# Kernel tuning notes

Hardware: AMD Instinct MI355X
Metric: run time of the kernel (lower is better)

## Reference

```python
import jax, jax.numpy as jnp
import numpy as np

B, T, C = 1, 2048, 1024
H = 16
HD = C // H  # 64
K = 8
EPS = 1e-6
NEG = -1.0e9


def apply_rotary_emb(x, cos, sin):
    # x: (B,T,H,HD), cos/sin: (T, HD//2)
    x1, x2 = jnp.split(x, 2, axis=-1)
    c = cos[None, :, None, :]
    s = sin[None, :, None, :]
    return jnp.concatenate([x1 * c - x2 * s, x1 * s + x2 * c], axis=-1)


def rms_norm(x):
    return x * jax.lax.rsqrt(jnp.mean(jnp.square(x), axis=-1, keepdims=True) + EPS)


def setup_inputs() -> dict:
    key = jax.random.key(0)
    ks = jax.random.split(key, 8)
    x = jax.random.normal(ks[0], (B, T, C), dtype=jnp.float32)
    # standard RoPE tables
    inv_freq = 1.0 / (10000.0 ** (np.arange(0, HD, 2, dtype=np.float32) / HD))
    t = np.arange(T, dtype=np.float32)
    freqs = np.outer(t, inv_freq)  # (T, HD//2)
    cos = jnp.asarray(np.cos(freqs), dtype=jnp.float32)
    sin = jnp.asarray(np.sin(freqs), dtype=jnp.float32)
    std = 0.02
    Wq = std * jax.random.normal(ks[1], (C, C), dtype=jnp.float32)
    Wk = std * jax.random.normal(ks[2], (C, C), dtype=jnp.float32)
    Wv = std * jax.random.normal(ks[3], (C, C), dtype=jnp.float32)
    Wproj = std * jax.random.normal(ks[4], (C, C), dtype=jnp.float32)
    Wdq = jax.random.normal(ks[5], (C, K), dtype=jnp.float32) / np.sqrt(C)
    Wdk = jax.random.normal(ks[6], (C, K), dtype=jnp.float32) / np.sqrt(C)
    return {"x": x, "cos": cos, "sin": sin, "Wq": Wq, "Wk": Wk, "Wv": Wv,
            "Wproj": Wproj, "Wdq": Wdq, "Wdk": Wdk}


def reference(x, cos, sin, Wq, Wk, Wv, Wproj, Wdq, Wdk):
    b, t, c = x.shape
    q = (x @ Wq).reshape(b, t, H, HD)
    k = (x @ Wk).reshape(b, t, H, HD)
    v = (x @ Wv).reshape(b, t, H, HD)
    q = rms_norm(apply_rotary_emb(q, cos, sin))
    k = rms_norm(apply_rotary_emb(k, cos, sin))

    # digit projections (identical for every head in the source module)
    qd = x @ Wdq  # (B,T,K)
    kd = x @ Wdk  # (B,T,K)
    matches = qd[:, :, None, :] == kd[:, None, :, :]  # (B,Tq,Tk,K)
    prefix = jnp.cumprod(matches.astype(jnp.int32), axis=-1)
    lcp = jnp.sum(prefix, axis=-1)  # (B,Tq,Tk)
    lcp_mask = lcp >= (K - 1)

    causal = jnp.tril(jnp.ones((t, t), dtype=bool))
    combined = causal[None, None, :, :] & lcp_mask[:, None, :, :]  # (B,1->H,Tq,Tk)

    scale = 1.0 / jnp.sqrt(jnp.asarray(HD, x.dtype))
    scores = jnp.einsum('bqhd,bkhd->bhqk', q * scale, k)
    scores = jnp.where(combined, scores, NEG)
    w = jax.nn.softmax(scores, axis=-1)
    y = jnp.einsum('bhqk,bkhd->bqhd', w, v).reshape(b, t, c)
    return y @ Wproj
```

## Files before the change

### kernel.cpp

```cpp
#include <hip/hip_runtime.h>
#include <math.h>

#define T_DIM 2048
#define C_DIM 1024
#define H_NUM 16
#define HD_DIM 64
#define K_LCP 8
#define NEG_VAL -1.0e9f
#define NBLK 256

typedef __bf16 bf16;
typedef __bf16 bf16x4 __attribute__((ext_vector_type(4)));
typedef __bf16 bf16x8 __attribute__((ext_vector_type(8)));
typedef float f32x4 __attribute__((ext_vector_type(4)));
typedef unsigned long long u64;

#define ALOAD(p) __hip_atomic_load((p), __ATOMIC_RELAXED, __HIP_MEMORY_SCOPE_AGENT)
#define ASTORE(p, v) \
  __hip_atomic_store((p), (v), __ATOMIC_RELAXED, __HIP_MEMORY_SCOPE_AGENT)

__device__ __forceinline__ u64 pk2(float lo, float hi) {
  return (u64)__float_as_uint(lo) | ((u64)__float_as_uint(hi) << 32);
}
__device__ __forceinline__ float upk_lo(u64 u) {
  return __uint_as_float((unsigned)u);
}
__device__ __forceinline__ float upk_hi(u64 u) {
  return __uint_as_float((unsigned)(u >> 32));
}

struct Prm {
  const float *x, *cosT, *sinT, *Wq, *Wk, *Wv, *Wproj, *Wdq, *Wdk;
  float* out;
  bf16 *xb, *wqt, *wkt, *wvt, *wpt, *qB, *kB, *vB;
  float *qd, *kd, *vtsum, *partial;
  int *tilemask, *allmask;
  u64* maskbits;
  float *vmean, *rowout;
  int* flags;
  int* bars;
};

__device__ __forceinline__ void gbar(int* bars, int slot, bool fence) {
  __syncthreads();
  if (threadIdx.x == 0) {
    if (fence) __threadfence();
    int* B = bars + slot * 32;
    const int g = blockIdx.x >> 5;
    int old = __hip_atomic_fetch_add(&B[1 + g], 1, __ATOMIC_RELAXED,
                                     __HIP_MEMORY_SCOPE_AGENT);
    if (old == 31) {
      __hip_atomic_fetch_add(&B[0], 1, __ATOMIC_RELAXED,
                             __HIP_MEMORY_SCOPE_AGENT);
      while (__hip_atomic_load(&B[0], __ATOMIC_RELAXED,
                               __HIP_MEMORY_SCOPE_AGENT) < 8)
        __builtin_amdgcn_s_sleep(8);
      ASTORE(&B[10 + g], 1);
    } else {
      while (ALOAD(&B[10 + g]) == 0) __builtin_amdgcn_s_sleep(8);
    }
    if (fence) __threadfence();
  }
  __syncthreads();
}

template <int TMt, int MI, int NA>
__device__ void gemm_body(bf16* As, bf16* Bs, const bf16* A, const bf16* Bt,
                          void* Cv, int bx, int by, int z, int mode,
                          const float* cosT, const float* sinT, float* vtsum) {
  const int tid = threadIdx.x;
  const int Kd = C_DIM, N = C_DIM;
  const int bm = by * TMt;
  const int bn = bx * 128;
  const int wave = tid >> 6, lane = tid & 63;
  const int lr = lane >> 2;
  const int lc = (lane & 3) * 8;
  bf16* gA = (bf16*)(A + (size_t)(bm + wave * 16 * NA + lr) * Kd + lc);
  bf16* gB = (bf16*)(Bt + (size_t)(bn + wave * 32 + lr) * Kd + lc);
  bf16* lA = As + wave * 512 * NA;
  bf16* lB = Bs + wave * 1024;
  const int wr = (wave >> 1) * (MI * 16);
  const int wc = (wave & 1) * 64;
  const int fm = lane & 15;
  const int fk_ = (lane >> 4) * 8;

  f32x4 acc[MI][4] = {};
  for (int k0 = 0; k0 < Kd; k0 += 32) {
    __syncthreads();
#pragma unroll
    for (int u = 0; u < NA; ++u)
      __builtin_amdgcn_global_load_lds(
          (__attribute__((address_space(1))) void*)(gA + (size_t)u * 16 * Kd + k0),
          (__attribute__((address_space(3))) void*)(lA + u * 512), 16, 0, 0);
#pragma unroll
    for (int u = 0; u < 2; ++u)
      __builtin_amdgcn_global_load_lds(
          (__attribute__((address_space(1))) void*)(gB + (size_t)u * 16 * Kd + k0),
          (__attribute__((address_space(3))) void*)(lB + u * 512), 16, 0, 0);
    __syncthreads();
    bf16x8 af[MI], bfr[4];
#pragma unroll
    for (int i = 0; i < MI; ++i)
      af[i] = *(const bf16x8*)(As + (size_t)(wr + i * 16 + fm) * 32 + fk_);
#pragma unroll
    for (int j = 0; j < 4; ++j)
      bfr[j] = *(const bf16x8*)(Bs + (size_t)(wc + j * 16 + fm) * 32 + fk_);
#pragma unroll
    for (int i = 0; i < MI; ++i)
#pragma unroll
      for (int j = 0; j < 4; ++j)
        acc[i][j] = __builtin_amdgcn_mfma_f32_16x16x32_bf16(af[i], bfr[j],
                                                            acc[i][j], 0, 0, 0);
  }
  const int cq = (lane >> 4) * 4;
  if (mode && z < 2) {
    bf16* C = (bf16*)Cv;
#pragma unroll
    for (int i = 0; i < MI; ++i)
#pragma unroll
      for (int r = 0; r < 4; ++r) {
        const int t = bm + wr + i * 16 + cq + r;
        float c0 = cosT[(size_t)t * 32 + fm], s0 = sinT[(size_t)t * 32 + fm];
        float c1 = cosT[(size_t)t * 32 + 16 + fm];
        float s1 = sinT[(size_t)t * 32 + 16 + fm];
        float a0 = acc[i][0][r], a1 = acc[i][1][r];
        float a2 = acc[i][2][r], a3 = acc[i][3][r];
        float o0 = a0 * c0 - a2 * s0, o2 = a0 * s0 + a2 * c0;
        float o1 = a1 * c1 - a3 * s1, o3 = a1 * s1 + a3 * c1;
        float ss = o0 * o0 + o1 * o1 + o2 * o2 + o3 * o3;
        ss += __shfl_xor(ss, 1);
        ss += __shfl_xor(ss, 2);
        ss += __shfl_xor(ss, 4);
        ss += __shfl_xor(ss, 8);
        float rn = 1.0f / sqrtf(ss * (1.0f / 64.0f) + 1e-6f);
        size_t base = (size_t)t * N + bn + wc + fm;
        C[base + 0] = (bf16)(o0 * rn);
        C[base + 16] = (bf16)(o1 * rn);
        C[base + 32] = (bf16)(o2 * rn);
        C[base + 48] = (bf16)(o3 * rn);
      }
  } else if (mode) {
    bf16* C = (bf16*)Cv;
#pragma unroll
    for (int i = 0; i < MI; ++i)
#pragma unroll
      for (int r = 0; r < 4; ++r) {
        size_t base = (size_t)(bm + wr + i * 16 + cq + r) * N + bn + wc + fm;
#pragma unroll
        for (int j = 0; j < 4; ++j) C[base + j * 16] = (bf16)acc[i][j][r];
      }
    const int kt = (bm + wr) >> 6;
#pragma unroll
    for (int j = 0; j < 4; ++j) {
      float s = 0.f;
#pragma unroll
      for (int i = 0; i < MI; ++i)
#pragma unroll
        for (int r = 0; r < 4; ++r) s += acc[i][j][r];
      s += __shfl_xor(s, 16);
      s += __shfl_xor(s, 32);
      if ((lane >> 4) == 0)
        vtsum[(size_t)kt * C_DIM + bn + wc + j * 16 + fm] = s;
    }
  } else {
    float* C = (float*)Cv;
#pragma unroll
    for (int i = 0; i < MI; ++i)
#pragma unroll
      for (int r = 0; r < 4; ++r) {
        size_t base = (size_t)(bm + wr + i * 16 + cq + r) * N + bn + wc + fm;
#pragma unroll
        for (int j = 0; j < 4; ++j) C[base + j * 16] = acc[i][j][r];
      }
  }
}

__device__ inline void write_vmean16(const float* vmp, bf16* yp) {
  f32x4 a0 = ((const f32x4*)vmp)[0];
  f32x4 a1 = ((const f32x4*)vmp)[1];
  f32x4 a2 = ((const f32x4*)vmp)[2];
  f32x4 a3 = ((const f32x4*)vmp)[3];
  bf16x8 o0 = {(bf16)a0[0], (bf16)a0[1], (bf16)a0[2], (bf16)a0[3],
               (bf16)a1[0], (bf16)a1[1], (bf16)a1[2], (bf16)a1[3]};
  bf16x8 o1 = {(bf16)a2[0], (bf16)a2[1], (bf16)a2[2], (bf16)a2[3],
               (bf16)a3[0], (bf16)a3[1], (bf16)a3[2], (bf16)a3[3]};
  *(bf16x8*)yp = o0;
  *(bf16x8*)(yp + 8) = o1;
}

__device__ void attn_body(int q64, int h, const bf16* q, const bf16* k,
                          const bf16* v, const float* vtsum,
                          const float* vmean, const u64* maskbits,
                          const int* tilemask, const int* allmask,
                          const int* pneed, bf16* y, char* smem) {
  bf16 (*vsT)[72] = (bf16(*)[72])smem;
  bf16 (*ps)[16][72] = (bf16(*)[16][72])(smem + 9216);
  int (*tmS)[32] = (int(*)[32])(smem + 18432);
  const int q0 = q64 * 64;
  const int tid = threadIdx.x;
  const int wv = tid >> 6;
  const int lane = tid & 63;
  const int qb0 = q0 >> 4;

  const int a0 = allmask[qb0 + 0], a1 = allmask[qb0 + 1];
  const int a2 = allmask[qb0 + 2], a3 = allmask[qb0 + 3];
  const int pn = pneed[q0 >> 6];
  if (a0 & a1 & a2 & a3) {
    if (pn) {
      const int row = tid >> 2, d0 = (tid & 3) * 16;
      write_vmean16(vmean + h * HD_DIM + d0,
                    y + (size_t)(q0 + row) * C_DIM + h * HD_DIM + d0);
    }
    return;
  }
  const int w_active = !((wv == 0) ? a0 : (wv == 1) ? a1 : (wv == 2) ? a2 : a3);

  if (tid < 128)
    tmS[tid >> 5][tid & 31] = tilemask[(size_t)(qb0 + (tid >> 5)) * 32 + (tid & 31)];

  if (!w_active && pn) {
    const int row = wv * 16 + (lane >> 2), d0 = (lane & 3) * 16;
    write_vmean16(vmean + h * HD_DIM + d0,
                  y + (size_t)(q0 + row) * C_DIM + h * HD_DIM + d0);
  }

  const int fm = lane & 15;
  const int fk = (lane >> 4) * 8;
  bf16x8 aq0 = {}, aq1 = {};
  if (w_active) {
    const bf16* qp = q + (size_t)(q0 + wv * 16 + fm) * C_DIM + h * HD_DIM;
    aq0 = *(const bf16x8*)(qp + fk);
    aq1 = *(const bf16x8*)(qp + 32 + fk);
  }
  __syncthreads();

  float m[4] = {-INFINITY, -INFINITY, -INFINITY, -INFINITY};
  float l[4] = {0.f, 0.f, 0.f, 0.f};
  f32x4 out[4] = {};

  for (int kt = 0; kt < T_DIM / 64; ++kt) {
    const int need = tmS[0][kt] | tmS[1][kt] | tmS[2][kt] | tmS[3][kt];
    const int k0 = kt * 64;
    if (need) {
      __syncthreads();
      {
        const int row = tid & 63, d0 = (tid >> 6) * 16;
        const bf16* vp = v + (size_t)(k0 + row) * C_DIM + h * HD_DIM + d0;
        bf16x8 v0 = *(const bf16x8*)(vp);
        bf16x8 v1 = *(const bf16x8*)(vp + 8);
#pragma unroll
        for (int i = 0; i < 8; ++i) vsT[d0 + i][row] = v0[i];
#pragma unroll
        for (int i = 0; i < 8; ++i) vsT[d0 + 8 + i][row] = v1[i];
      }
      __syncthreads();
    }
    if (!w_active) continue;
    if (tmS[wv][kt]) {
      u64 mwr[4];
#pragma unroll
      for (int r = 0; r < 4; ++r)
        mwr[r] = maskbits[(size_t)(q0 + wv * 16 + (lane >> 4) * 4 + r) * 32 + kt] >> fm;
      f32x4 s[4] = {};
#pragma unroll
      for (int j = 0; j < 4; ++j) {
        const bf16* kp = k + (size_t)(k0 + j * 16 + fm) * C_DIM + h * HD_DIM;
        bf16x8 bk0 = *(const bf16x8*)(kp + fk);
        bf16x8 bk1 = *(const bf16x8*)(kp + 32 + fk);
        s[j] = __builtin_amdgcn_mfma_f32_16x16x32_bf16(aq0, bk0, s[j], 0, 0, 0);
        s[j] = __builtin_amdgcn_mfma_f32_16x16x32_bf16(aq1, bk1, s[j], 0, 0, 0);
      }
      float xv[4][4];
      float tmax[4] = {NEG_VAL, NEG_VAL, NEG_VAL, NEG_VAL};
#pragma unroll
      for (int j = 0; j < 4; ++j)
#pragma unroll
        for (int r = 0; r < 4; ++r) {
          float val = ((mwr[r] >> (16 * j)) & 1ull) ? s[j][r] * 0.125f : NEG_VAL;
          xv[j][r] = val;
          tmax[r] = fmaxf(tmax[r], val);
        }
#pragma unroll
      for (int r = 0; r < 4; ++r) {
#pragma unroll
        for (int off = 1; off < 16; off <<= 1)
          tmax[r] = fmaxf(tmax[r], __shfl_xor(tmax[r], off));
      }
      float alpha[4], lsum[4] = {0.f, 0.f, 0.f, 0.f};
#pragma unroll
      for (int r = 0; r < 4; ++r) {
        float mn = fmaxf(m[r], tmax[r]);
        alpha[r] = __expf(m[r] - mn);
        m[r] = mn;
      }
#pragma unroll
      for (int j = 0; j < 4; ++j)
#pragma unroll
        for (int r = 0; r < 4; ++r) {
          float pp = __expf(xv[j][r] - m[r]);
          lsum[r] += pp;
          ps[wv][(lane >> 4) * 4 + r][j * 16 + fm] = (bf16)pp;
        }
#pragma unroll
      for (int r = 0; r < 4; ++r) {
#pragma unroll
        for (int off = 1; off < 16; off <<= 1) lsum[r] += __shfl_xor(lsum[r], off);
        l[r] = l[r] * alpha[r] + lsum[r];
      }
#pragma unroll
      for (int jd = 0; jd < 4; ++jd)
#pragma unroll
        for (int r = 0; r < 4; ++r) out[jd][r] *= alpha[r];
      bf16x8 pa0 = *(const bf16x8*)&ps[wv][fm][fk];
      bf16x8 pa1 = *(const bf16x8*)&ps[wv][fm][32 + fk];
#pragma unroll
      for (int jd = 0; jd < 4; ++jd) {
        bf16x8 bv0 = *(const bf16x8*)&vsT[jd * 16 + fm][fk];
        bf16x8 bv1 = *(const bf16x8*)&vsT[jd * 16 + fm][32 + fk];
        out[jd] = __builtin_amdgcn_mfma_f32_16x16x32_bf16(pa0, bv0, out[jd], 0, 0, 0);
        out[jd] = __builtin_amdgcn_mfma_f32_16x16x32_bf16(pa1, bv1, out[jd], 0, 0, 0);
      }
    } else {
      int needu = (m[0] <= NEG_VAL) | (m[1] <= NEG_VAL) | (m[2] <= NEG_VAL) |
                  (m[3] <= NEG_VAL);
      if (needu) {
#pragma unroll
        for (int jd = 0; jd < 4; ++jd) {
          float vt = vtsum[(size_t)kt * C_DIM + h * HD_DIM + jd * 16 + fm];
#pragma unroll
          for (int r = 0; r < 4; ++r)
            if (m[r] <= NEG_VAL) out[jd][r] += vt;
        }
#pragma unroll
        for (int r = 0; r < 4; ++r)
          if (m[r] <= NEG_VAL) {
            m[r] = NEG_VAL;
            l[r] += 64.f;
          }
      }
    }
  }

  if (w_active) {
#pragma unroll
    for (int r = 0; r < 4; ++r) {
      float inv_l = 1.0f / l[r];
      bf16* yp = y + (size_t)(q0 + wv * 16 + (lane >> 4) * 4 + r) * C_DIM +
                 h * HD_DIM + fm;
#pragma unroll
      for (int jd = 0; jd < 4; ++jd) yp[jd * 16] = (bf16)(out[jd][r] * inv_l);
    }
  }
}

__global__ __launch_bounds__(256, 2) void mono(Prm p) {
  const int gid = blockIdx.x;
  const int tid = threadIdx.x;
  const int wave = tid >> 6, lane = tid & 63;
  __shared__ __align__(16) char smem[19456];

  int* qneed = p.flags;
  int* kneed = p.flags + 16;
  int* vneed = p.flags + 32;
  int* pneed = p.flags + 48;
  int* anyfl = p.flags + 80;

  for (int rr = 0; rr < 2; ++rr) {
    const int t = gid * 8 + rr * 4 + wave;
    const float* xp = p.x + (size_t)t * C_DIM;
    float aq[8] = {}, ak[8] = {};
#pragma unroll
    for (int i = 0; i < 16; ++i) {
      const int c = i * 64 + lane;
      float xv = xp[c];
      float4 wq0 = *(const float4*)(p.Wdq + (size_t)c * K_LCP);
      float4 wq1 = *(const float4*)(p.Wdq + (size_t)c * K_LCP + 4);
      float4 wk0 = *(const float4*)(p.Wdk + (size_t)c * K_LCP);
      float4 wk1 = *(const float4*)(p.Wdk + (size_t)c * K_LCP + 4);
      aq[0] = fmaf(xv, wq0.x, aq[0]); aq[1] = fmaf(xv, wq0.y, aq[1]);
      aq[2] = fmaf(xv, wq0.z, aq[2]); aq[3] = fmaf(xv, wq0.w, aq[3]);
      aq[4] = fmaf(xv, wq1.x, aq[4]); aq[5] = fmaf(xv, wq1.y, aq[5]);
      aq[6] = fmaf(xv, wq1.z, aq[6]); aq[7] = fmaf(xv, wq1.w, aq[7]);
      ak[0] = fmaf(xv, wk0.x, ak[0]); ak[1] = fmaf(xv, wk0.y, ak[1]);
      ak[2] = fmaf(xv, wk0.z, ak[2]); ak[3] = fmaf(xv, wk0.w, ak[3]);
      ak[4] = fmaf(xv, wk1.x, ak[4]); ak[5] = fmaf(xv, wk1.y, ak[5]);
      ak[6] = fmaf(xv, wk1.z, ak[6]); ak[7] = fmaf(xv, wk1.w, ak[7]);
    }
#pragma unroll
    for (int j = 0; j < 8; ++j) {
#pragma unroll
      for (int off = 32; off >= 1; off >>= 1) {
        aq[j] += __shfl_xor(aq[j], off);
        ak[j] += __shfl_xor(ak[j], off);
      }
    }
    if (lane == 0) {
      u64* qdp = (u64*)(p.qd + (size_t)t * K_LCP);
      u64* kdp = (u64*)(p.kd + (size_t)t * K_LCP);
#pragma unroll
      for (int j = 0; j < 4; ++j) {
        ASTORE(qdp + j, pk2(aq[2 * j], aq[2 * j + 1]));
        ASTORE(kdp + j, pk2(ak[2 * j], ak[2 * j + 1]));
      }
    }
  }
  if (gid < 32) {
    f32x4 s = {0.f, 0.f, 0.f, 0.f};
    for (int r = 0; r < 64; ++r)
      s += ((const f32x4*)(p.x + (size_t)(gid * 64 + r) * C_DIM))[tid];
    u64* dst = (u64*)(p.partial + (size_t)gid * C_DIM) + tid * 2;
    ASTORE(dst + 0, pk2(s[0], s[1]));
    ASTORE(dst + 1, pk2(s[2], s[3]));
  }
  gbar(p.bars, 0, false);

  if (gid < 128) {
    const int qb = gid;
    float (*qds)[K_LCP] = (float(*)[K_LCP])smem;
    int* tm = (int*)(smem + 512);
    if (tid < 32) tm[tid] = 0;
    if (tid < 64) {
      u64 u = ALOAD((u64*)(p.qd + (size_t)qb * 16 * K_LCP) + tid);
      qds[tid >> 2][(tid & 3) * 2 + 0] = upk_lo(u);
      qds[tid >> 2][(tid & 3) * 2 + 1] = upk_hi(u);
    }
    __syncthreads();
    const int kmax = qb * 16 + 15;
    for (int it = 0; it < 8; ++it) {
      const int kbase = it * 256 + wave * 64;
      if (kbase > kmax) break;
      const int key = kbase + lane;
      const u64* kp = (const u64*)(p.kd + (size_t)key * K_LCP);
      float kv[K_LCP];
#pragma unroll
      for (int jj = 0; jj < 4; ++jj) {
        u64 u = ALOAD(kp + jj);
        kv[2 * jj + 0] = upk_lo(u);
        kv[2 * jj + 1] = upk_hi(u);
      }
      const int grp = it * 4 + wave;
      u64 anyb = 0ull;
#pragma unroll
      for (int ql = 0; ql < 16; ++ql) {
        const int qg = qb * 16 + ql;
        bool pr = (key <= qg) & (qds[ql][0] == kv[0]) & (qds[ql][1] == kv[1]) &
                  (qds[ql][2] == kv[2]) & (qds[ql][3] == kv[3]) &
                  (qds[ql][4] == kv[4]) & (qds[ql][5] == kv[5]) &
                  (qds[ql][6] == kv[6]);
        u64 b = __ballot(pr);
        anyb |= b;
        if (lane == 0) ASTORE(p.maskbits + (size_t)qg * 32 + grp, b);
      }
      if (lane == 0 && anyb) tm[grp] = 1;
    }
    __syncthreads();
    int anytm = 0;
#pragma unroll
    for (int i = 0; i < 32; ++i) anytm |= tm[i];
    if (tid < 32) ASTORE(p.tilemask + qb * 32 + tid, tm[tid]);
    if (tid == 0) ASTORE(p.allmask + qb, !anytm);
    if (anytm) {
      if (tid < 32) {
        if (tm[tid]) atomicOr(&kneed[tid >> 1], 1);
        atomicOr(&vneed[tid >> 1], 1);
      }
      if (tid == 0) {
        atomicOr(&qneed[qb >> 3], 1);
        atomicOr(&pneed[qb >> 2], 1);
        atomicOr(anyfl, 1);
      }
    }
  } else if (gid < 192) {
    const int b = gid - 128;
    const int cs = (b >> 4) * 256;
    const int jb = (b & 15) * 64;
    float* xm = (float*)smem;
    f32x4 (*xr)[64] = (f32x4(*)[64])(smem + 1024);
    float (*red)[64] = (float(*)[64])(smem + 5120);
    const int pq = tid >> 6, t6 = tid & 63;
    {
      f32x4 s = {0.f, 0.f, 0.f, 0.f};
      for (int g = pq * 8; g < pq * 8 + 8; ++g) {
        const u64* pp = (const u64*)(p.partial + (size_t)g * C_DIM + cs) + t6 * 2;
        u64 a = ALOAD(pp + 0), bu = ALOAD(pp + 1);
        s[0] += upk_lo(a); s[1] += upk_hi(a);
        s[2] += upk_lo(bu); s[3] += upk_hi(bu);
      }
      xr[pq][t6] = s;
      __syncthreads();
      if (pq == 0) {
        f32x4 t = (xr[0][t6] + xr[1][t6]) + (xr[2][t6] + xr[3][t6]);
        t *= (1.0f / 2048.0f);
        *(f32x4*)&xm[t6 * 4] = t;
      }
      __syncthreads();
    }
    const int j = jb + t6;
    float acc = 0.f;
    for (int c = pq * 64; c < pq * 64 + 64; ++c)
      acc = fmaf(xm[c], p.Wv[(size_t)(cs + c) * C_DIM + j], acc);
    red[pq][t6] = acc;
    __syncthreads();
    if (tid < 64)
      atomicAdd(&p.vmean[jb + tid],
                (red[0][tid] + red[1][tid]) + (red[2][tid] + red[3][tid]));
  }
  gbar(p.bars, 1, false);

  __shared__ int anyS;
  if (tid == 0) anyS = ALOAD(anyfl);
  __syncthreads();
  const int any = anyS;

  if (!any) {
    float* xm = (float*)smem;
    float (*red)[64] = (float(*)[64])(smem + 4096);
    float* rs = (float*)(smem + 5120);
    const int pq = tid >> 6, t6 = tid & 63;
#pragma unroll
    for (int kk = 0; kk < 4; ++kk)
      xm[tid * 4 + kk] = ALOAD(p.vmean + tid * 4 + kk);
    __syncthreads();
    const int jb = (gid & 15) * 64;
    float acc = 0.f;
    for (int c = pq * 256; c < pq * 256 + 256; ++c)
      acc = fmaf(xm[c], p.Wproj[(size_t)c * C_DIM + jb + t6], acc);
    red[pq][t6] = acc;
    __syncthreads();
    if (tid < 64)
      rs[tid] = (red[0][tid] + red[1][tid]) + (red[2][tid] + red[3][tid]);
    __syncthreads();
    const int r0 = (gid >> 4) * 128;
    f32x4 v4 = *(const f32x4*)&rs[(tid & 15) * 4];
#pragma unroll
    for (int kk = 0; kk < 8; ++kk) {
      const int row = r0 + (tid >> 4) + kk * 16;
      *(f32x4*)(p.out + (size_t)row * C_DIM + jb + (tid & 15) * 4) = v4;
    }
    return;
  }

  if (tid == 0) __threadfence();
  __syncthreads();
  for (int rr = 0; rr < 8; ++rr) {
    const int t = gid * 8 + rr;
    float4 f = *(const float4*)(p.x + (size_t)t * C_DIM + tid * 4);
    bf16x4 o = {(bf16)f.x, (bf16)f.y, (bf16)f.z, (bf16)f.w};
    *(bf16x4*)(p.xb + (size_t)t * C_DIM + tid * 4) = o;
  }
  {
    bf16 (*tile)[67] = (bf16(*)[67])smem;
    for (int it = 0; it < 4; ++it) {
      const int idx = gid * 4 + it;
      const int z = idx >> 8;
      const float* W = (z == 0) ? p.Wq : (z == 1) ? p.Wk : (z == 2) ? p.Wv : p.Wproj;
      bf16* O = (z == 0) ? p.wqt : (z == 1) ? p.wkt : (z == 2) ? p.wvt : p.wpt;
      const int rem = idx & 255;
      const int bk = (rem >> 4) * 64;
      const int bn = (rem & 15) * 64;
      __syncthreads();
      {
        const int r = tid >> 2;
        const int c0 = (tid & 3) * 16;
        const float* src = W + (size_t)(bk + r) * C_DIM + bn + c0;
#pragma unroll
        for (int t = 0; t < 16; t += 4) {
          float4 f = *(const float4*)(src + t);
          tile[r][c0 + t + 0] = (bf16)f.x;
          tile[r][c0 + t + 1] = (bf16)f.y;
          tile[r][c0 + t + 2] = (bf16)f.z;
          tile[r][c0 + t + 3] = (bf16)f.w;
        }
      }
      __syncthreads();
      {
        const int n = tid >> 2;
        const int k0 = (tid & 3) * 16;
        bf16x8 lo, hi;
#pragma unroll
        for (int j = 0; j < 8; ++j) lo[j] = tile[k0 + j][n];
#pragma unroll
        for (int j = 0; j < 8; ++j) hi[j] = tile[k0 + 8 + j][n];
        bf16* dst = O + (size_t)(bn + n) * C_DIM + bk + k0;
        *(bf16x8*)dst = lo;
        *(bf16x8*)(dst + 8) = hi;
      }
    }
  }
  if (gid < 64) {
    __syncthreads();
    float* xm = (float*)smem;
    float (*red)[64] = (float(*)[64])(smem + 1024);
    const int cs = (gid >> 4) * 256;
    const int jb = (gid & 15) * 64;
    const int pq = tid >> 6, t6 = tid & 63;
    xm[tid] = ALOAD(p.vmean + cs + tid);
    __syncthreads();
    const int j = jb + t6;
    float acc = 0.f;
    for (int c = pq * 64; c < pq * 64 + 64; ++c)
      acc = fmaf(xm[c], p.Wproj[(size_t)(cs + c) * C_DIM + j], acc);
    red[pq][t6] = acc;
    __syncthreads();
    if (tid < 64)
      atomicAdd(&p.rowout[jb + tid],
                (red[0][tid] + red[1][tid]) + (red[2][tid] + red[3][tid]));
  }
  gbar(p.bars, 3, true);

  {
    bf16* As = (bf16*)smem;
    bf16* Bs = (bf16*)(smem + 8192);
    for (int v = gid; v < 384; v += 256) {
      __syncthreads();
      const int z = v >> 7, r = v & 127, by = r >> 3, bx = r & 7;
      const int* f = (z == 0) ? qneed : (z == 1) ? kneed : vneed;
      if (!f[by]) continue;
      const bf16* Bt = (z == 0) ? p.wqt : (z == 1) ? p.wkt : p.wvt;
      void* C = (z == 0) ? (void*)p.qB : (z == 1) ? (void*)p.kB : (void*)p.vB;
      gemm_body<128, 4, 2>(As, Bs, p.xb, Bt, C, bx, by, z, 1, p.cosT, p.sinT,
                           p.vtsum);
    }
  }
  gbar(p.bars, 4, true);

  for (int v = gid; v < 512; v += 256) {
    __syncthreads();
    attn_body(v & 31, v >> 5, p.qB, p.kB, p.vB, p.vtsum, p.vmean, p.maskbits,
              p.tilemask, p.allmask, pneed, p.xb , smem);
  }
  gbar(p.bars, 5, true);

  {
    bf16* As = (bf16*)smem;
    bf16* Bs = (bf16*)(smem + 8192);
    const int by = gid >> 3, bx = gid & 7;
    if (pneed[by])
      gemm_body<64, 2, 1>(As, Bs, p.xb , p.wpt, (void*)p.out, bx, by, 2,
                          0, p.cosT, p.sinT, nullptr);
    f32x4 v4;
    v4[0] = ALOAD(p.rowout + tid * 4 + 0);
    v4[1] = ALOAD(p.rowout + tid * 4 + 1);
    v4[2] = ALOAD(p.rowout + tid * 4 + 2);
    v4[3] = ALOAD(p.rowout + tid * 4 + 3);
#pragma unroll
    for (int r = 0; r < 8; ++r) {
      const int row = gid * 8 + r;
      if (!pneed[row >> 6])
        ((f32x4*)(p.out + (size_t)row * C_DIM))[tid] = v4;
    }
  }
}

extern "C" void kernel_launch(void* const* d_in, const int* in_sizes, int n_in,
                              void* d_out, int out_size, void* d_ws, size_t ws_size,
                              hipStream_t stream) {
  char* ws = (char*)d_ws;
  const size_t TC2 = (size_t)T_DIM * C_DIM * 2;
  const size_t CC2 = (size_t)C_DIM * C_DIM * 2;
  Prm p;
  p.x = (const float*)d_in[0];
  p.cosT = (const float*)d_in[1];
  p.sinT = (const float*)d_in[2];
  p.Wq = (const float*)d_in[3];
  p.Wk = (const float*)d_in[4];
  p.Wv = (const float*)d_in[5];
  p.Wproj = (const float*)d_in[6];
  p.Wdq = (const float*)d_in[7];
  p.Wdk = (const float*)d_in[8];
  p.out = (float*)d_out;
  p.xb = (bf16*)(ws + 0);
  p.wqt = (bf16*)(ws + TC2);
  p.wkt = (bf16*)(ws + TC2 + CC2);
  p.wvt = (bf16*)(ws + TC2 + 2 * CC2);
  p.wpt = (bf16*)(ws + TC2 + 3 * CC2);
  p.qB = (bf16*)(ws + TC2 + 4 * CC2);
  p.kB = (bf16*)(ws + 2 * TC2 + 4 * CC2);
  p.vB = (bf16*)(ws + 3 * TC2 + 4 * CC2);
  char* p2 = ws + 4 * TC2 + 4 * CC2;
  p.qd = (float*)p2;      p2 += (size_t)T_DIM * K_LCP * 4;
  p.kd = (float*)p2;      p2 += (size_t)T_DIM * K_LCP * 4;
  p.vtsum = (float*)p2;   p2 += 32 * C_DIM * 4;
  p.partial = (float*)p2; p2 += 32 * C_DIM * 4;
  p.tilemask = (int*)p2;  p2 += (T_DIM / 16) * 32 * 4;
  p.allmask = (int*)p2;   p2 += (T_DIM / 16) * 4;
  p.maskbits = (u64*)p2;  p2 += (size_t)T_DIM * 32 * 8;
  char* ctrl = p2;
  p.vmean = (float*)p2;   p2 += C_DIM * 4;
  p.rowout = (float*)p2;  p2 += C_DIM * 4;
  p.flags = (int*)p2;     p2 += 128 * 4;
  p.bars = (int*)p2;      p2 += 6 * 32 * 4;
  const size_t ctrl_bytes = (size_t)(p2 - ctrl);

  hipMemsetAsync(ctrl, 0, ctrl_bytes, stream);
  mono<<<NBLK, 256, 0, stream>>>(p);
}
```

Measured before the change: 136.0 us.

## Prefetch Wproj/Wv into cache before barrier and vectorize fallback matvecs

Idle blocks in the first phase now touch their slices of Wproj and Wv so those weights are already in L2/MALL when the later mean-value matvecs run. The V-mean and projection matvecs are rewritten to use float4 loads, with 16 row-partitions reduced through shared memory instead of 4 scalar partitions. The barrier spin sleep is shortened, and the LCP mask loop bound is computed directly. These changes target latency on the fast path where the whole mask is empty, at the cost of extra memory traffic during phase 0.

Measured after the change: 137.5 us. Within noise of the previous version (+1.1%).

```diff
diff --git a/kernel.cpp b/kernel.cpp
--- a/kernel.cpp
+++ b/kernel.cpp
@@ -57,7 +57,7 @@
         __builtin_amdgcn_s_sleep(8);
       ASTORE(&B[10 + g], 1);
     } else {
-      while (ALOAD(&B[10 + g]) == 0) __builtin_amdgcn_s_sleep(8);
+      while (ALOAD(&B[10 + g]) == 0) __builtin_amdgcn_s_sleep(2);
     }
     if (fence) __threadfence();
   }
@@ -411,6 +411,21 @@
     u64* dst = (u64*)(p.partial + (size_t)gid * C_DIM) + tid * 2;
     ASTORE(dst + 0, pk2(s[0], s[1]));
     ASTORE(dst + 1, pk2(s[2], s[3]));
+  } else {
+    const int jbp = (gid & 15) * 64;
+    float accp = 0.f;
+#pragma unroll
+    for (int k = 0; k < 16; ++k)
+      accp += p.Wproj[(size_t)((tid >> 2) + k * 64) * C_DIM + jbp + (tid & 3) * 16];
+    asm volatile("" ::"v"(accp));
+    if (gid >= 128 && gid < 192) {
+      const int b = gid - 128, cs = (b >> 4) * 256, jbv = (b & 15) * 64;
+      float accv = 0.f;
+#pragma unroll
+      for (int k = 0; k < 4; ++k)
+        accv += p.Wv[(size_t)(cs + (tid >> 2) + k * 64) * C_DIM + jbv + (tid & 3) * 16];
+      asm volatile("" ::"v"(accv));
+    }
   }
   gbar(p.bars, 0, false);
 
@@ -425,11 +440,9 @@
       qds[tid >> 2][(tid & 3) * 2 + 1] = upk_hi(u);
     }
     __syncthreads();
-    const int kmax = qb * 16 + 15;
-    for (int it = 0; it < 8; ++it) {
-      const int kbase = it * 256 + wave * 64;
-      if (kbase > kmax) break;
-      const int key = kbase + lane;
+    const int nit = (qb >> 4) + 1;
+    for (int it = 0; it < nit; ++it) {
+      const int key = it * 256 + wave * 64 + lane;
       const u64* kp = (const u64*)(p.kd + (size_t)key * K_LCP);
       float kv[K_LCP];
 #pragma unroll
@@ -476,34 +489,40 @@
     const int jb = (b & 15) * 64;
     float* xm = (float*)smem;
     f32x4 (*xr)[64] = (f32x4(*)[64])(smem + 1024);
-    float (*red)[64] = (float(*)[64])(smem + 5120);
-    const int pq = tid >> 6, t6 = tid & 63;
+    f32x4 (*red)[16] = (f32x4(*)[16])(smem + 5120);
+    const int pg = tid >> 6, t6 = tid & 63;
     {
       f32x4 s = {0.f, 0.f, 0.f, 0.f};
-      for (int g = pq * 8; g < pq * 8 + 8; ++g) {
+      for (int g = pg * 8; g < pg * 8 + 8; ++g) {
         const u64* pp = (const u64*)(p.partial + (size_t)g * C_DIM + cs) + t6 * 2;
         u64 a = ALOAD(pp + 0), bu = ALOAD(pp + 1);
         s[0] += upk_lo(a); s[1] += upk_hi(a);
         s[2] += upk_lo(bu); s[3] += upk_hi(bu);
       }
-      xr[pq][t6] = s;
+      xr[pg][t6] = s;
       __syncthreads();
-      if (pq == 0) {
+      if (pg == 0) {
         f32x4 t = (xr[0][t6] + xr[1][t6]) + (xr[2][t6] + xr[3][t6]);
         t *= (1.0f / 2048.0f);
         *(f32x4*)&xm[t6 * 4] = t;
       }
       __syncthreads();
     }
-    const int j = jb + t6;
-    float acc = 0.f;
-    for (int c = pq * 64; c < pq * 64 + 64; ++c)
-      acc = fmaf(xm[c], p.Wv[(size_t)(cs + c) * C_DIM + j], acc);
-    red[pq][t6] = acc;
-    __syncthreads();
-    if (tid < 64)
-      atomicAdd(&p.vmean[jb + tid],
-                (red[0][tid] + red[1][tid]) + (red[2][tid] + red[3][tid]));
+    const int jg = tid & 15, pq = tid >> 4;
+    f32x4 acc = {0.f, 0.f, 0.f, 0.f};
+#pragma unroll 4
+    for (int i = 0; i < 16; ++i) {
+      const int c = pq * 16 + i;
+      acc += xm[c] * *(const f32x4*)(p.Wv + (size_t)(cs + c) * C_DIM + jb + jg * 4);
+    }
+    red[pq][jg] = acc;
+    __syncthreads();
+    if (tid < 64) {
+      float s = 0.f;
+#pragma unroll
+      for (int q = 0; q < 16; ++q) s += red[q][tid >> 2][tid & 3];
+      atomicAdd(&p.vmean[jb + tid], s);
+    }
   }
   gbar(p.bars, 1, false);
 
@@ -514,21 +533,28 @@
 
   if (!any) {
     float* xm = (float*)smem;
-    float (*red)[64] = (float(*)[64])(smem + 4096);
-    float* rs = (float*)(smem + 5120);
-    const int pq = tid >> 6, t6 = tid & 63;
+    f32x4 (*red)[16] = (f32x4(*)[16])(smem + 4096);
+    float* rs = (float*)(smem + 8192);
 #pragma unroll
     for (int kk = 0; kk < 4; ++kk)
       xm[tid * 4 + kk] = ALOAD(p.vmean + tid * 4 + kk);
     __syncthreads();
     const int jb = (gid & 15) * 64;
-    float acc = 0.f;
-    for (int c = pq * 256; c < pq * 256 + 256; ++c)
-      acc = fmaf(xm[c], p.Wproj[(size_t)c * C_DIM + jb + t6], acc);
-    red[pq][t6] = acc;
-    __syncthreads();
-    if (tid < 64)
-      rs[tid] = (red[0][tid] + red[1][tid]) + (red[2][tid] + red[3][tid]);
+    const int jg = tid & 15, pq = tid >> 4;
+    f32x4 acc = {0.f, 0.f, 0.f, 0.f};
+#pragma unroll 8
+    for (int i = 0; i < 64; ++i) {
+      const int c = pq * 64 + i;
+      acc += xm[c] * *(const f32x4*)(p.Wproj + (size_t)c * C_DIM + jb + jg * 4);
+    }
+    red[pq][jg] = acc;
+    __syncthreads();
+    if (tid < 64) {
+      float s = 0.f;
+#pragma unroll
+      for (int q = 0; q < 16; ++q) s += red[q][tid >> 2][tid & 3];
+      rs[tid] = s;
+    }
     __syncthreads();
     const int r0 = (gid >> 4) * 128;
     f32x4 v4 = *(const f32x4*)&rs[(tid & 15) * 4];
```
